# Performance work log

Hardware: AMD Instinct MI355X
Metric: run time of the kernel (lower is better)

The kernel has to match this reference:

```python
import jax, jax.numpy as jnp
import numpy as np

B, N_P, N_S, D, H = 8, 512, 512, 512, 8
HD = D // H
SCALE = HD ** -0.5


def setup_inputs() -> dict:
    key = jax.random.key(0)
    ks = jax.random.split(key, 16)
    init = lambda k, shape, fan_in: jax.random.normal(k, shape, jnp.float32) * (1.0 / np.sqrt(fan_in))
    return {
        "piece_embeds": jax.random.normal(ks[0], (B, N_P, D), jnp.float32),
        "slot_embeds": jax.random.normal(ks[1], (B, N_S, D), jnp.float32),
        "mask": jax.random.randint(ks[2], (B, N_P, N_S), 0, 2, jnp.int32),
        "spatial_bias": jax.random.normal(ks[3], (B, N_P, N_S), jnp.float32),
        "Wq": init(ks[4], (D, D), D), "bq": jnp.zeros((D,), jnp.float32),
        "Wk": init(ks[5], (D, D), D), "bk": jnp.zeros((D,), jnp.float32),
        "Wv": init(ks[6], (D, D), D), "bv": jnp.zeros((D,), jnp.float32),
        "Wo": init(ks[7], (D, D), D), "bo": jnp.zeros((D,), jnp.float32),
        "Wc": init(ks[8], (2 * D,), 2 * D), "bc": jnp.zeros((), jnp.float32),
        "Wval": init(ks[9], (D,), D), "bval": jnp.zeros((), jnp.float32),
    }


def reference(piece_embeds, slot_embeds, mask, spatial_bias,
              Wq, bq, Wk, bk, Wv, bv, Wo, bo, Wc, bc, Wval, bval):
    Bv, Np, Dv = piece_embeds.shape
    Ns = slot_embeds.shape[1]
    Q = (piece_embeds @ Wq + bq).reshape(Bv, Np, H, HD)
    K = (slot_embeds @ Wk + bk).reshape(Bv, Ns, H, HD)
    V = (slot_embeds @ Wv + bv).reshape(Bv, Ns, H, HD)
    # per-head scores, scaled, then averaged over heads (non-standard)
    scores = jnp.einsum('bphd,bshd->bps', Q, K) * (SCALE / H)
    scores = scores + spatial_bias
    scores = jnp.where(mask == 0, jnp.float32(-1e9), scores)
    attn_probs = jax.nn.softmax(scores, axis=-1)  # dropout is identity at eval
    # the original expand*mul*sum over [B,Np,Ns,H,HD] == this contraction
    attn_output = jnp.einsum('bps,bshd->bphd', attn_probs, V).reshape(Bv, Np, Dv)
    output = attn_output @ Wo + bo
    value = (output.mean(axis=1) @ Wval + bval)[:, None]  # [B,1]
    # concat-linear over pairs == split-weight GEMMs with broadcast add
    Wc_p, Wc_s = Wc[:Dv], Wc[Dv:]
    compatibility = (piece_embeds @ Wc_p)[:, :, None] + (slot_embeds @ Wc_s)[:, None, :] + bc
    return scores, value, compatibility
```

## Files before the change

kernel.cpp:

```cpp
#include <hip/hip_runtime.h>
#include <math.h>

#define NP 512
#define NS 512
#define DD 512
#define INV64 0.015625f
#define NEGBIG -1000000000.0f
#define LOG2E 1.4426950408889634f

#define WS_MTBF   0
#define WS_TBF    131072
#define WS_PBF    1179648
#define WS_SBF    2228224
#define WS_WV     3538944
#define WS_U      3539456
#define WS_WQBK   3539968
#define WS_WKBQ   3540480
#define WS_VV     3540992
#define WS_A      3545088
#define WS_E      3549184
#define WS_CP     3553280
#define WS_CS     3557376
#define WS_Z      3561472
#define WS_W      3565568
#define WS_SC     3569664
#define WS_CNT    3569680

#define OUT_SCORES 0
#define OUT_VALUE  2097152
#define OUT_COMP   2097160

typedef short bf16x8 __attribute__((ext_vector_type(8)));
typedef float f32x4 __attribute__((ext_vector_type(4)));

__device__ __forceinline__ short f2bf(float f) {
  unsigned u = __builtin_bit_cast(unsigned, f);
  u += 0x7fffu + ((u >> 16) & 1u);
  return (short)(u >> 16);
}

__device__ __forceinline__ bf16x8 cvt8(float4 a, float4 b) {
  bf16x8 o;
  o[0] = f2bf(a.x); o[1] = f2bf(a.y); o[2] = f2bf(a.z); o[3] = f2bf(a.w);
  o[4] = f2bf(b.x); o[5] = f2bf(b.y); o[6] = f2bf(b.z); o[7] = f2bf(b.w);
  return o;
}

__device__ __forceinline__ void async_copy16(const void* g, void* l) {
  __builtin_amdgcn_global_load_lds(
      (const __attribute__((address_space(1))) unsigned int*)g,
      (__attribute__((address_space(3))) unsigned int*)l, 16, 0, 0);
}

__device__ __forceinline__ float dot8(float4 a0, float4 a1, float4 b0, float4 b1) {
  return a0.x * b0.x + a0.y * b0.y + a0.z * b0.z + a0.w * b0.w +
         a1.x * b1.x + a1.y * b1.y + a1.z * b1.z + a1.w * b1.w;
}

__device__ __forceinline__ float wave_red(float s) {
#pragma unroll
  for (int o = 32; o; o >>= 1) s += __shfl_xor(s, o);
  return s;
}

__device__ inline float wave_dot512(const float* __restrict__ x,
                                    const float* __restrict__ y, int lane) {
  float4 x0 = *(const float4*)&x[lane * 8];
  float4 x1 = *(const float4*)&x[lane * 8 + 4];
  float4 y0 = *(const float4*)&y[lane * 8];
  float4 y1 = *(const float4*)&y[lane * 8 + 4];
  return wave_red(dot8(x0, x1, y0, y1));
}

__global__ __launch_bounds__(256) void kAM(
    const float* __restrict__ Wo, const float* __restrict__ Wval,
    const float* __restrict__ Wq, const float* __restrict__ bk,
    const float* __restrict__ Wk, const float* __restrict__ bq,
    const float* __restrict__ bo, const float* __restrict__ bval,
    float* __restrict__ ws, short* __restrict__ mtb) {
  __shared__ alignas(16) short Asw[2][64 * 72];
  __shared__ alignas(16) short Bsw[2][64 * 72];
  int blk = blockIdx.x;
  if (blk < 385) {
    int wid = blk * 4 + (threadIdx.x >> 6);
    int lane = threadIdx.x & 63;
    if (wid >= 1538) return;
    const float *x, *y;
    float* dst;
    float extra = 0.f;
    int r = wid & 511;
    if (wid < 512)        { x = Wo + (size_t)r * DD; y = Wval; dst = ws + WS_WV + r; }
    else if (wid < 1024)  { x = Wq + (size_t)r * DD; y = bk;   dst = ws + WS_WQBK + r; }
    else if (wid < 1536)  { x = Wk + (size_t)r * DD; y = bq;   dst = ws + WS_WKBQ + r; }
    else if (wid == 1536) { x = bo; y = Wval; dst = ws + WS_SC + 1; extra = *bval; }
    else                  { x = bq; y = bk;   dst = ws + WS_SC + 2; }
    float s = wave_dot512(x, y, lane);
    if (lane == 0) *dst = s + extra;
    return;
  }
  int gb = blk - 385;
  const int m0 = (gb & 7) * 64, n0 = (gb >> 3) * 64;
  const int wave = threadIdx.x >> 6, lane = threadIdx.x & 63;
  const int wr = wave >> 1, wc = wave & 1;
  const int li = lane & 15, g = lane >> 4;
  const int arow = threadIdx.x >> 2, aseg = threadIdx.x & 3;
  f32x4 acc[2][2] = {};

  auto stage = [&](int bufi, int k0) {
    const float* sa = Wk + (size_t)(m0 + arow) * DD + k0 + aseg * 16;
    float4 a0 = *(const float4*)sa, a1 = *(const float4*)(sa + 4);
    float4 a2 = *(const float4*)(sa + 8), a3 = *(const float4*)(sa + 12);
    const float* sb = Wq + (size_t)(n0 + arow) * DD + k0 + aseg * 16;
    float4 b0 = *(const float4*)sb, b1 = *(const float4*)(sb + 4);
    float4 b2 = *(const float4*)(sb + 8), b3 = *(const float4*)(sb + 12);
    *(bf16x8*)&Asw[bufi][arow * 72 + aseg * 16] = cvt8(a0, a1);
    *(bf16x8*)&Asw[bufi][arow * 72 + aseg * 16 + 8] = cvt8(a2, a3);
    *(bf16x8*)&Bsw[bufi][arow * 72 + aseg * 16] = cvt8(b0, b1);
    *(bf16x8*)&Bsw[bufi][arow * 72 + aseg * 16 + 8] = cvt8(b2, b3);
  };

  stage(0, 0);
  __syncthreads();
  int buf = 0;
  for (int k0 = 0; k0 < DD; k0 += 64) {
    if (k0 + 64 < DD) stage(buf ^ 1, k0 + 64);
    bf16x8 af[2][2], bfv[2][2];
#pragma unroll
    for (int kk = 0; kk < 2; ++kk) {
#pragma unroll
      for (int am = 0; am < 2; ++am)
        af[am][kk] = *(const bf16x8*)&Asw[buf][(wr * 32 + am * 16 + li) * 72 + kk * 32 + g * 8];
#pragma unroll
      for (int bn = 0; bn < 2; ++bn)
        bfv[bn][kk] = *(const bf16x8*)&Bsw[buf][(wc * 32 + bn * 16 + li) * 72 + kk * 32 + g * 8];
    }
#pragma unroll
    for (int kk = 0; kk < 2; ++kk)
#pragma unroll
      for (int am = 0; am < 2; ++am)
#pragma unroll
        for (int bn = 0; bn < 2; ++bn)
          acc[am][bn] = __builtin_amdgcn_mfma_f32_16x16x32_bf16(
              af[am][kk], bfv[bn][kk], acc[am][bn], 0, 0, 0);
    __syncthreads();
    buf ^= 1;
  }
#pragma unroll
  for (int am = 0; am < 2; ++am)
#pragma unroll
    for (int i = 0; i < 4; ++i) {
      int grow = m0 + wr * 32 + am * 16 + g * 4 + i;
#pragma unroll
      for (int bn = 0; bn < 2; ++bn) {
        int gcol = n0 + wc * 32 + bn * 16 + li;
        mtb[(size_t)grow * DD + gcol] = f2bf(acc[am][bn][i]);
      }
    }
}

__global__ __launch_bounds__(256) void kCp(
    const float* __restrict__ piece, const float* __restrict__ Wv,
    const float* __restrict__ bv, const float* __restrict__ Wc,
    float* __restrict__ ws, short* __restrict__ pbf, float* __restrict__ out) {
  int lane = threadIdx.x & 63;
  if (blockIdx.x < 1024) {
    int wid = blockIdx.x * 4 + (threadIdx.x >> 6);
    const float* row = piece + (size_t)wid * DD;
    float4 x0 = *(const float4*)&row[lane * 8];
    float4 x1 = *(const float4*)&row[lane * 8 + 4];
    bf16x8 o;
    o[0] = f2bf(x0.x); o[1] = f2bf(x0.y); o[2] = f2bf(x0.z); o[3] = f2bf(x0.w);
    o[4] = f2bf(x1.x); o[5] = f2bf(x1.y); o[6] = f2bf(x1.z); o[7] = f2bf(x1.w);
    *(bf16x8*)&pbf[(size_t)wid * DD + lane * 8] = o;
    const float* y = ws + WS_WQBK;
    float4 y0 = *(const float4*)&y[lane * 8];
    float4 y1 = *(const float4*)&y[lane * 8 + 4];
    float4 c0 = *(const float4*)&Wc[lane * 8];
    float4 c1 = *(const float4*)&Wc[lane * 8 + 4];
    float da = wave_red(dot8(x0, x1, y0, y1));
    float dc = wave_red(dot8(x0, x1, c0, c1));
    if (lane == 0) { ws[WS_A + wid] = da; ws[WS_CP + wid] = dc; }
  } else if (blockIdx.x < 1153) {
    int wid = ((int)blockIdx.x - 1024) * 4 + (threadIdx.x >> 6);
    if (wid > 512) return;
    if (wid < 512) {
      float s = wave_dot512(Wv + (size_t)wid * DD, ws + WS_WV, lane);
      if (lane == 0) ws[WS_U + wid] = s;
    } else {
      float s = wave_dot512(bv, ws + WS_WV, lane);
      if (lane == 0) ws[WS_SC + 0] = s;
    }
  } else {
    float4 zz = make_float4(0.f, 0.f, 0.f, 0.f);
#pragma unroll
    for (int k = 0; k < 8; ++k)
      *(float4*)&ws[WS_Z + (threadIdx.x * 8 + k) * 4] = zz;
    if (threadIdx.x < 64) ((unsigned*)(ws + WS_CNT))[threadIdx.x] = 0u;
    if (threadIdx.x < 8) out[OUT_VALUE + threadIdx.x] = ws[WS_SC + 1];
  }
}

template <int MODE>
__global__ __launch_bounds__(256) void k64(
    const short* __restrict__ A, const short* __restrict__ B,
    short* __restrict__ Cb, const float* __restrict__ slotp,
    const float* __restrict__ Wc, float* __restrict__ ws,
    const float* __restrict__ sbias, const int* __restrict__ maskp,
    const float* __restrict__ bc, float* __restrict__ out,
    short* __restrict__ sbf) {
  __shared__ alignas(16) short SH[4][4096];
  __shared__ unsigned tick;
  const int wave = threadIdx.x >> 6, lane = threadIdx.x & 63;
  const int id = blockIdx.x;

  if (MODE == 1 && id >= 512) {
    int wid = (id - 512) * 4 + wave;
    const float* row = slotp + (size_t)wid * DD;
    float4 x0 = *(const float4*)&row[lane * 8];
    float4 x1 = *(const float4*)&row[lane * 8 + 4];
    bf16x8 o;
    o[0] = f2bf(x0.x); o[1] = f2bf(x0.y); o[2] = f2bf(x0.z); o[3] = f2bf(x0.w);
    o[4] = f2bf(x1.x); o[5] = f2bf(x1.y); o[6] = f2bf(x1.z); o[7] = f2bf(x1.w);
    *(bf16x8*)&sbf[(size_t)wid * DD + lane * 8] = o;
    const float* y = ws + WS_WKBQ;
    float4 y0 = *(const float4*)&y[lane * 8];
    float4 y1 = *(const float4*)&y[lane * 8 + 4];
    const float* u = ws + WS_U;
    float4 u0 = *(const float4*)&u[lane * 8];
    float4 u1 = *(const float4*)&u[lane * 8 + 4];
    const float* c = Wc + DD;
    float4 c0 = *(const float4*)&c[lane * 8];
    float4 c1 = *(const float4*)&c[lane * 8 + 4];
    float de = wave_red(dot8(x0, x1, y0, y1));
    float dv = wave_red(dot8(x0, x1, u0, u1));
    float dc = wave_red(dot8(x0, x1, c0, c1));
    if (lane == 0) {
      ws[WS_E + wid] = de;
      ws[WS_VV + wid] = dv + ws[WS_SC + 0];
      ws[WS_CS + wid] = dc;
    }
    return;
  }

  const int wr = wave >> 1, wc = wave & 1;
  const int li = lane & 15, g = lane >> 4;
  int b = 0, m0, n0;
  if (MODE == 1) { m0 = (id & 63) * 64; n0 = (id >> 6) * 64; }
  else           { b = id & 7; m0 = ((id >> 6) & 7) * 64; n0 = ((id >> 3) & 7) * 64; }
  const short* Ab = A + (size_t)b * NP * DD;
  const short* Bb = B + (size_t)b * NS * DD;
  f32x4 acc[2][2] = {};
  float4 sb4r[4];
  int4 mk4r[4];
  const int er = threadIdx.x >> 2, eq = threadIdx.x & 3;
  const size_t ebase = ((size_t)b * NP + m0 + er) * NS + n0 + eq * 16;

  auto stage = [&](int bufi, int k0) {
#pragma unroll
    for (int h = 0; h < 2; ++h) {
      int s = h * 256 + threadIdx.x;
      int row = s >> 3;
      int gsrc = (s & 7) ^ (row & 7);
      async_copy16(Ab + (size_t)(m0 + row) * DD + k0 + gsrc * 8, &SH[bufi][s * 8]);
      async_copy16(Bb + (size_t)(n0 + row) * DD + k0 + gsrc * 8, &SH[2 + bufi][s * 8]);
    }
  };

  stage(0, 0);
  __syncthreads();
  int buf = 0;
  for (int k0 = 0; k0 < DD; k0 += 64) {
    if (k0 + 64 < DD) stage(buf ^ 1, k0 + 64);
    if (MODE == 2) {
      if (k0 == 256) {
#pragma unroll
        for (int h = 0; h < 4; ++h)
          sb4r[h] = *(const float4*)&sbias[ebase + h * 4];
      } else if (k0 == 384) {
#pragma unroll
        for (int h = 0; h < 4; ++h)
          mk4r[h] = *(const int4*)&maskp[ebase + h * 4];
      }
    }
    bf16x8 af[2][2], bfv[2][2];
#pragma unroll
    for (int kk = 0; kk < 2; ++kk) {
#pragma unroll
      for (int am = 0; am < 2; ++am) {
        int row = wr * 32 + am * 16 + li;
        af[am][kk] = *(const bf16x8*)&SH[buf][(row * 8 + ((kk * 4 + g) ^ (row & 7))) * 8];
      }
#pragma unroll
      for (int bn = 0; bn < 2; ++bn) {
        int row = wc * 32 + bn * 16 + li;
        bfv[bn][kk] = *(const bf16x8*)&SH[2 + buf][(row * 8 + ((kk * 4 + g) ^ (row & 7))) * 8];
      }
    }
#pragma unroll
    for (int kk = 0; kk < 2; ++kk)
#pragma unroll
      for (int am = 0; am < 2; ++am)
#pragma unroll
        for (int bn = 0; bn < 2; ++bn)
          acc[am][bn] = __builtin_amdgcn_mfma_f32_16x16x32_bf16(
              af[am][kk], bfv[bn][kk], acc[am][bn], 0, 0, 0);
    if (k0 + 64 < DD) {
      __syncthreads();
      buf ^= 1;
    }
  }
  __syncthreads();

  if (MODE == 1) {
    short* cs = &SH[0][0];
#pragma unroll
    for (int am = 0; am < 2; ++am)
#pragma unroll
      for (int i = 0; i < 4; ++i) {
        int row = wr * 32 + am * 16 + g * 4 + i;
#pragma unroll
        for (int bn = 0; bn < 2; ++bn)
          cs[row * 68 + wc * 32 + bn * 16 + li] = f2bf(acc[am][bn][i]);
      }
    __syncthreads();
    int r = threadIdx.x >> 2, q = threadIdx.x & 3;
#pragma unroll
    for (int h = 0; h < 2; ++h) {
      bf16x8 v = *(const bf16x8*)&cs[r * 68 + q * 16 + h * 8];
      *(bf16x8*)&Cb[(size_t)(m0 + r) * DD + n0 + q * 16 + h * 8] = v;
    }
  } else {
    float* cf = (float*)&SH[0][0];
#pragma unroll
    for (int am = 0; am < 2; ++am)
#pragma unroll
      for (int i = 0; i < 4; ++i) {
        int row = wr * 32 + am * 16 + g * 4 + i;
#pragma unroll
        for (int bn = 0; bn < 2; ++bn)
          cf[row * 68 + wc * 32 + bn * 16 + li] = acc[am][bn][i];
      }
    __syncthreads();
    const float sbb = ws[WS_SC + 2];
    const float bcv = *bc;
    int p = m0 + er;
    float av = ws[WS_A + b * NP + p] + sbb;
    float cpv = ws[WS_CP + b * NP + p] + bcv;
    float zp = 0.f, wp = 0.f;
#pragma unroll
    for (int h = 0; h < 4; ++h) {
      int c = eq * 16 + h * 4;
      int scol = n0 + c;
      size_t idx = ebase + h * 4;
      float4 a4 = *(const float4*)&cf[er * 68 + c];
      float4 sb4 = sb4r[h];
      int4 mk4 = mk4r[h];
      float4 e4 = *(const float4*)&ws[WS_E + b * NS + scol];
      float4 vv4 = *(const float4*)&ws[WS_VV + b * NS + scol];
      float4 cs4 = *(const float4*)&ws[WS_CS + b * NS + scol];
      float4 v;
      v.x = (mk4.x == 0) ? NEGBIG : fmaf(a4.x + av + e4.x, INV64, sb4.x);
      v.y = (mk4.y == 0) ? NEGBIG : fmaf(a4.y + av + e4.y, INV64, sb4.y);
      v.z = (mk4.z == 0) ? NEGBIG : fmaf(a4.z + av + e4.z, INV64, sb4.z);
      v.w = (mk4.w == 0) ? NEGBIG : fmaf(a4.w + av + e4.w, INV64, sb4.w);
      *(float4*)&out[OUT_SCORES + idx] = v;
      float e;
      e = exp2f(v.x * LOG2E); zp += e; wp += e * vv4.x;
      e = exp2f(v.y * LOG2E); zp += e; wp += e * vv4.y;
      e = exp2f(v.z * LOG2E); zp += e; wp += e * vv4.z;
      e = exp2f(v.w * LOG2E); zp += e; wp += e * vv4.w;
      float4 cm = make_float4(cpv + cs4.x, cpv + cs4.y, cpv + cs4.z, cpv + cs4.w);
      *(float4*)&out[OUT_COMP + idx] = cm;
    }
    zp += __shfl_xor(zp, 1); zp += __shfl_xor(zp, 2);
    wp += __shfl_xor(wp, 1); wp += __shfl_xor(wp, 2);
    if (eq == 0) {
      atomicAdd(&ws[WS_Z + b * NP + p], zp);
      atomicAdd(&ws[WS_W + b * NP + p], wp);
    }
    __syncthreads();
    if (threadIdx.x == 0)
      tick = atomicAdd((unsigned*)(ws + WS_CNT) + (b * 8 + ((id >> 6) & 7)), 1u);
    __syncthreads();
    if (tick == 7 && threadIdx.x < 64) {
      int pr = m0 + threadIdx.x;
      float zz = atomicAdd(&ws[WS_Z + b * NP + pr], 0.0f);
      float ww = atomicAdd(&ws[WS_W + b * NP + pr], 0.0f);
      float v = wave_red(ww / zz);
      if (threadIdx.x == 0) atomicAdd(&out[OUT_VALUE + b], v * (1.0f / NP));
    }
  }
}

extern "C" void kernel_launch(void* const* d_in, const int* in_sizes, int n_in,
                              void* d_out, int out_size, void* d_ws,
                              size_t ws_size, hipStream_t stream) {
  const float* piece = (const float*)d_in[0];
  const float* slot = (const float*)d_in[1];
  const int* mask = (const int*)d_in[2];
  const float* sbias = (const float*)d_in[3];
  const float* Wq = (const float*)d_in[4];
  const float* bq = (const float*)d_in[5];
  const float* Wk = (const float*)d_in[6];
  const float* bk = (const float*)d_in[7];
  const float* Wv = (const float*)d_in[8];
  const float* bv = (const float*)d_in[9];
  const float* Wo = (const float*)d_in[10];
  const float* bo = (const float*)d_in[11];
  const float* Wc = (const float*)d_in[12];
  const float* bc = (const float*)d_in[13];
  const float* Wval = (const float*)d_in[14];
  const float* bval = (const float*)d_in[15];
  float* out = (float*)d_out;
  float* ws = (float*)d_ws;

  short* mtb = (short*)(ws + WS_MTBF);
  short* tbf = (short*)(ws + WS_TBF);
  short* pbf = (short*)(ws + WS_PBF);
  short* sbf = (short*)(ws + WS_SBF);

  hipLaunchKernelGGL(kAM, dim3(449), dim3(256), 0, stream,
                     Wo, Wval, Wq, bk, Wk, bq, bo, bval, ws, mtb);
  hipLaunchKernelGGL(kCp, dim3(1154), dim3(256), 0, stream,
                     piece, Wv, bv, Wc, ws, pbf, out);
  hipLaunchKernelGGL((k64<1>), dim3(1536), dim3(256), 0, stream,
                     pbf, mtb, tbf, slot, Wc, ws,
                     (const float*)nullptr, (const int*)nullptr,
                     (const float*)nullptr, (float*)nullptr, sbf);
  hipLaunchKernelGGL((k64<2>), dim3(512), dim3(256), 0, stream,
                     tbf, sbf, (short*)nullptr, (const float*)nullptr,
                     (const float*)nullptr, ws, sbias, mask, bc, out,
                     (short*)nullptr);
}
```

Baseline: 43.11 us.

## Fuse fp32-to-bf16 input conversion and row dot products into GEMM kernels

```diff
diff --git a/kernel.cpp b/kernel.cpp
--- a/kernel.cpp
+++ b/kernel.cpp
@@ -10,21 +10,16 @@
 
 #define WS_MTBF   0
 #define WS_TBF    131072
-#define WS_PBF    1179648
-#define WS_SBF    2228224
-#define WS_WV     3538944
-#define WS_U      3539456
-#define WS_WQBK   3539968
-#define WS_WKBQ   3540480
-#define WS_VV     3540992
-#define WS_A      3545088
-#define WS_E      3549184
-#define WS_CP     3553280
-#define WS_CS     3557376
-#define WS_Z      3561472
-#define WS_W      3565568
-#define WS_SC     3569664
-#define WS_CNT    3569680
+#define WS_WV     1179648
+#define WS_U      1180160
+#define WS_WQBK   1180672
+#define WS_WKBQ   1181184
+#define WS_A      1181696
+#define WS_CP     1185792
+#define WS_Z      1189888
+#define WS_W      1193984
+#define WS_SC     1198080
+#define WS_CNT    1198096
 
 #define OUT_SCORES 0
 #define OUT_VALUE  2097152
@@ -158,111 +153,66 @@
     }
 }
 
-__global__ __launch_bounds__(256) void kCp(
-    const float* __restrict__ piece, const float* __restrict__ Wv,
-    const float* __restrict__ bv, const float* __restrict__ Wc,
-    float* __restrict__ ws, short* __restrict__ pbf, float* __restrict__ out) {
-  int lane = threadIdx.x & 63;
-  if (blockIdx.x < 1024) {
-    int wid = blockIdx.x * 4 + (threadIdx.x >> 6);
-    const float* row = piece + (size_t)wid * DD;
-    float4 x0 = *(const float4*)&row[lane * 8];
-    float4 x1 = *(const float4*)&row[lane * 8 + 4];
-    bf16x8 o;
-    o[0] = f2bf(x0.x); o[1] = f2bf(x0.y); o[2] = f2bf(x0.z); o[3] = f2bf(x0.w);
-    o[4] = f2bf(x1.x); o[5] = f2bf(x1.y); o[6] = f2bf(x1.z); o[7] = f2bf(x1.w);
-    *(bf16x8*)&pbf[(size_t)wid * DD + lane * 8] = o;
-    const float* y = ws + WS_WQBK;
-    float4 y0 = *(const float4*)&y[lane * 8];
-    float4 y1 = *(const float4*)&y[lane * 8 + 4];
-    float4 c0 = *(const float4*)&Wc[lane * 8];
-    float4 c1 = *(const float4*)&Wc[lane * 8 + 4];
-    float da = wave_red(dot8(x0, x1, y0, y1));
-    float dc = wave_red(dot8(x0, x1, c0, c1));
-    if (lane == 0) { ws[WS_A + wid] = da; ws[WS_CP + wid] = dc; }
-  } else if (blockIdx.x < 1153) {
-    int wid = ((int)blockIdx.x - 1024) * 4 + (threadIdx.x >> 6);
-    if (wid > 512) return;
-    if (wid < 512) {
-      float s = wave_dot512(Wv + (size_t)wid * DD, ws + WS_WV, lane);
-      if (lane == 0) ws[WS_U + wid] = s;
+__global__ __launch_bounds__(256) void kT(
+    const float* __restrict__ piece, const short* __restrict__ mtb,
+    const float* __restrict__ Wv, const float* __restrict__ bv,
+    const float* __restrict__ Wc, float* __restrict__ ws,
+    short* __restrict__ tbf, float* __restrict__ out) {
+  __shared__ alignas(16) short Asw[2][64 * 72];
+  __shared__ alignas(16) short Bsg[2][64 * 64];
+  const int id = blockIdx.x;
+  const int wave = threadIdx.x >> 6, lane = threadIdx.x & 63;
+
+  if (id >= 512) {
+    if (id < 641) {
+      int wid = (id - 512) * 4 + wave;
+      if (wid > 512) return;
+      if (wid < 512) {
+        float s = wave_dot512(Wv + (size_t)wid * DD, ws + WS_WV, lane);
+        if (lane == 0) ws[WS_U + wid] = s;
+      } else {
+        float s = wave_dot512(bv, ws + WS_WV, lane);
+        if (lane == 0) ws[WS_SC + 0] = s;
+      }
     } else {
-      float s = wave_dot512(bv, ws + WS_WV, lane);
-      if (lane == 0) ws[WS_SC + 0] = s;
-    }
-  } else {
-    float4 zz = make_float4(0.f, 0.f, 0.f, 0.f);
-#pragma unroll
-    for (int k = 0; k < 8; ++k)
-      *(float4*)&ws[WS_Z + (threadIdx.x * 8 + k) * 4] = zz;
-    if (threadIdx.x < 64) ((unsigned*)(ws + WS_CNT))[threadIdx.x] = 0u;
-    if (threadIdx.x < 8) out[OUT_VALUE + threadIdx.x] = ws[WS_SC + 1];
-  }
-}
-
-template <int MODE>
-__global__ __launch_bounds__(256) void k64(
-    const short* __restrict__ A, const short* __restrict__ B,
-    short* __restrict__ Cb, const float* __restrict__ slotp,
-    const float* __restrict__ Wc, float* __restrict__ ws,
-    const float* __restrict__ sbias, const int* __restrict__ maskp,
-    const float* __restrict__ bc, float* __restrict__ out,
-    short* __restrict__ sbf) {
-  __shared__ alignas(16) short SH[4][4096];
-  __shared__ unsigned tick;
-  const int wave = threadIdx.x >> 6, lane = threadIdx.x & 63;
-  const int id = blockIdx.x;
-
-  if (MODE == 1 && id >= 512) {
-    int wid = (id - 512) * 4 + wave;
-    const float* row = slotp + (size_t)wid * DD;
-    float4 x0 = *(const float4*)&row[lane * 8];
-    float4 x1 = *(const float4*)&row[lane * 8 + 4];
-    bf16x8 o;
-    o[0] = f2bf(x0.x); o[1] = f2bf(x0.y); o[2] = f2bf(x0.z); o[3] = f2bf(x0.w);
-    o[4] = f2bf(x1.x); o[5] = f2bf(x1.y); o[6] = f2bf(x1.z); o[7] = f2bf(x1.w);
-    *(bf16x8*)&sbf[(size_t)wid * DD + lane * 8] = o;
-    const float* y = ws + WS_WKBQ;
-    float4 y0 = *(const float4*)&y[lane * 8];
-    float4 y1 = *(const float4*)&y[lane * 8 + 4];
-    const float* u = ws + WS_U;
-    float4 u0 = *(const float4*)&u[lane * 8];
-    float4 u1 = *(const float4*)&u[lane * 8 + 4];
-    const float* c = Wc + DD;
-    float4 c0 = *(const float4*)&c[lane * 8];
-    float4 c1 = *(const float4*)&c[lane * 8 + 4];
-    float de = wave_red(dot8(x0, x1, y0, y1));
-    float dv = wave_red(dot8(x0, x1, u0, u1));
-    float dc = wave_red(dot8(x0, x1, c0, c1));
-    if (lane == 0) {
-      ws[WS_E + wid] = de;
-      ws[WS_VV + wid] = dv + ws[WS_SC + 0];
-      ws[WS_CS + wid] = dc;
+      float4 zz = make_float4(0.f, 0.f, 0.f, 0.f);
+#pragma unroll
+      for (int k = 0; k < 8; ++k)
+        *(float4*)&ws[WS_Z + (threadIdx.x * 8 + k) * 4] = zz;
+      if (threadIdx.x < 64) ((unsigned*)(ws + WS_CNT))[threadIdx.x] = 0u;
+      if (threadIdx.x < 8) out[OUT_VALUE + threadIdx.x] = ws[WS_SC + 1];
     }
     return;
   }
 
   const int wr = wave >> 1, wc = wave & 1;
   const int li = lane & 15, g = lane >> 4;
-  int b = 0, m0, n0;
-  if (MODE == 1) { m0 = (id & 63) * 64; n0 = (id >> 6) * 64; }
-  else           { b = id & 7; m0 = ((id >> 6) & 7) * 64; n0 = ((id >> 3) & 7) * 64; }
-  const short* Ab = A + (size_t)b * NP * DD;
-  const short* Bb = B + (size_t)b * NS * DD;
+  const int m0 = (id & 63) * 64, n0 = (id >> 6) * 64;
+  const int arow = threadIdx.x >> 2, aseg = threadIdx.x & 3;
+  const bool do_dots = (n0 == 0);
+  float a_acc = 0.f, cp_acc = 0.f;
   f32x4 acc[2][2] = {};
-  float4 sb4r[4];
-  int4 mk4r[4];
-  const int er = threadIdx.x >> 2, eq = threadIdx.x & 3;
-  const size_t ebase = ((size_t)b * NP + m0 + er) * NS + n0 + eq * 16;
 
   auto stage = [&](int bufi, int k0) {
+    const float* sa = piece + (size_t)(m0 + arow) * DD + k0 + aseg * 16;
+    float4 a0 = *(const float4*)sa, a1 = *(const float4*)(sa + 4);
+    float4 a2 = *(const float4*)(sa + 8), a3 = *(const float4*)(sa + 12);
 #pragma unroll
     for (int h = 0; h < 2; ++h) {
       int s = h * 256 + threadIdx.x;
       int row = s >> 3;
       int gsrc = (s & 7) ^ (row & 7);
-      async_copy16(Ab + (size_t)(m0 + row) * DD + k0 + gsrc * 8, &SH[bufi][s * 8]);
-      async_copy16(Bb + (size_t)(n0 + row) * DD + k0 + gsrc * 8, &SH[2 + bufi][s * 8]);
+      async_copy16(mtb + (size_t)(n0 + row) * DD + k0 + gsrc * 8, &Bsg[bufi][s * 8]);
+    }
+    *(bf16x8*)&Asw[bufi][arow * 72 + aseg * 16] = cvt8(a0, a1);
+    *(bf16x8*)&Asw[bufi][arow * 72 + aseg * 16 + 8] = cvt8(a2, a3);
+    if (do_dots) {
+      const float* yq = ws + WS_WQBK + k0 + aseg * 16;
+      const float* yc = Wc + k0 + aseg * 16;
+      a_acc += dot8(a0, a1, *(const float4*)yq, *(const float4*)(yq + 4)) +
+               dot8(a2, a3, *(const float4*)(yq + 8), *(const float4*)(yq + 12));
+      cp_acc += dot8(a0, a1, *(const float4*)yc, *(const float4*)(yc + 4)) +
+                dot8(a2, a3, *(const float4*)(yc + 8), *(const float4*)(yc + 12));
     }
   };
 
@@ -271,29 +221,16 @@
   int buf = 0;
   for (int k0 = 0; k0 < DD; k0 += 64) {
     if (k0 + 64 < DD) stage(buf ^ 1, k0 + 64);
-    if (MODE == 2) {
-      if (k0 == 256) {
-#pragma unroll
-        for (int h = 0; h < 4; ++h)
-          sb4r[h] = *(const float4*)&sbias[ebase + h * 4];
-      } else if (k0 == 384) {
-#pragma unroll
-        for (int h = 0; h < 4; ++h)
-          mk4r[h] = *(const int4*)&maskp[ebase + h * 4];
-      }
-    }
     bf16x8 af[2][2], bfv[2][2];
 #pragma unroll
     for (int kk = 0; kk < 2; ++kk) {
 #pragma unroll
-      for (int am = 0; am < 2; ++am) {
-        int row = wr * 32 + am * 16 + li;
-        af[am][kk] = *(const bf16x8*)&SH[buf][(row * 8 + ((kk * 4 + g) ^ (row & 7))) * 8];
-      }
+      for (int am = 0; am < 2; ++am)
+        af[am][kk] = *(const bf16x8*)&Asw[buf][(wr * 32 + am * 16 + li) * 72 + kk * 32 + g * 8];
 #pragma unroll
       for (int bn = 0; bn < 2; ++bn) {
         int row = wc * 32 + bn * 16 + li;
-        bfv[bn][kk] = *(const bf16x8*)&SH[2 + buf][(row * 8 + ((kk * 4 + g) ^ (row & 7))) * 8];
+        bfv[bn][kk] = *(const bf16x8*)&Bsg[buf][(row * 8 + ((kk * 4 + g) ^ (row & 7))) * 8];
       }
     }
 #pragma unroll
@@ -309,86 +246,188 @@
       buf ^= 1;
     }
   }
-  __syncthreads();
-
-  if (MODE == 1) {
-    short* cs = &SH[0][0];
-#pragma unroll
-    for (int am = 0; am < 2; ++am)
-#pragma unroll
-      for (int i = 0; i < 4; ++i) {
-        int row = wr * 32 + am * 16 + g * 4 + i;
+  if (do_dots) {
+    a_acc += __shfl_xor(a_acc, 1);  a_acc += __shfl_xor(a_acc, 2);
+    cp_acc += __shfl_xor(cp_acc, 1); cp_acc += __shfl_xor(cp_acc, 2);
+    if (aseg == 0) {
+      ws[WS_A + m0 + arow] = a_acc;
+      ws[WS_CP + m0 + arow] = cp_acc;
+    }
+  }
+  __syncthreads();
+  short* cs = &Asw[0][0];
+#pragma unroll
+  for (int am = 0; am < 2; ++am)
+#pragma unroll
+    for (int i = 0; i < 4; ++i) {
+      int row = wr * 32 + am * 16 + g * 4 + i;
+#pragma unroll
+      for (int bn = 0; bn < 2; ++bn)
+        cs[row * 68 + wc * 32 + bn * 16 + li] = f2bf(acc[am][bn][i]);
+    }
+  __syncthreads();
+  int r = threadIdx.x >> 2, q = threadIdx.x & 3;
+#pragma unroll
+  for (int h = 0; h < 2; ++h) {
+    bf16x8 v = *(const bf16x8*)&cs[r * 68 + q * 16 + h * 8];
+    *(bf16x8*)&tbf[(size_t)(m0 + r) * DD + n0 + q * 16 + h * 8] = v;
+  }
+}
+
+__global__ __launch_bounds__(256) void kS(
+    const short* __restrict__ tbf, const float* __restrict__ slotp,
+    const float* __restrict__ Wc, float* __restrict__ ws,
+    const float* __restrict__ sbias, const int* __restrict__ maskp,
+    const float* __restrict__ bc, float* __restrict__ out) {
+  __shared__ alignas(16) short Asg[2][64 * 64];
+  __shared__ alignas(16) short Bsw[2][64 * 72];
+  __shared__ alignas(16) float e_l[64];
+  __shared__ alignas(16) float vv_l[64];
+  __shared__ alignas(16) float cs_l[64];
+  __shared__ unsigned tick;
+  const int id = blockIdx.x;
+  const int wave = threadIdx.x >> 6, lane = threadIdx.x & 63;
+  const int wr = wave >> 1, wc = wave & 1;
+  const int li = lane & 15, g = lane >> 4;
+  const int b = id & 7, m0 = ((id >> 6) & 7) * 64, n0 = ((id >> 3) & 7) * 64;
+  const short* Ab = tbf + (size_t)b * NP * DD;
+  const int brow = threadIdx.x >> 2, bseg = threadIdx.x & 3;
+  float e_acc = 0.f, vv_acc = 0.f, cs_acc = 0.f;
+  f32x4 acc[2][2] = {};
+  float4 sb4r[4];
+  int4 mk4r[4];
+  const int er = threadIdx.x >> 2, eq = threadIdx.x & 3;
+  const size_t ebase = ((size_t)b * NP + m0 + er) * NS + n0 + eq * 16;
+
+  auto stage = [&](int bufi, int k0) {
+    const float* sb = slotp + (size_t)(b * NS + n0 + brow) * DD + k0 + bseg * 16;
+    float4 b0 = *(const float4*)sb, b1 = *(const float4*)(sb + 4);
+    float4 b2 = *(const float4*)(sb + 8), b3 = *(const float4*)(sb + 12);
+#pragma unroll
+    for (int h = 0; h < 2; ++h) {
+      int s = h * 256 + threadIdx.x;
+      int row = s >> 3;
+      int gsrc = (s & 7) ^ (row & 7);
+      async_copy16(Ab + (size_t)(m0 + row) * DD + k0 + gsrc * 8, &Asg[bufi][s * 8]);
+    }
+    *(bf16x8*)&Bsw[bufi][brow * 72 + bseg * 16] = cvt8(b0, b1);
+    *(bf16x8*)&Bsw[bufi][brow * 72 + bseg * 16 + 8] = cvt8(b2, b3);
+    const float* yk = ws + WS_WKBQ + k0 + bseg * 16;
+    const float* yu = ws + WS_U + k0 + bseg * 16;
+    const float* yc = Wc + DD + k0 + bseg * 16;
+    e_acc += dot8(b0, b1, *(const float4*)yk, *(const float4*)(yk + 4)) +
+             dot8(b2, b3, *(const float4*)(yk + 8), *(const float4*)(yk + 12));
+    vv_acc += dot8(b0, b1, *(const float4*)yu, *(const float4*)(yu + 4)) +
+              dot8(b2, b3, *(const float4*)(yu + 8), *(const float4*)(yu + 12));
+    cs_acc += dot8(b0, b1, *(const float4*)yc, *(const float4*)(yc + 4)) +
+              dot8(b2, b3, *(const float4*)(yc + 8), *(const float4*)(yc + 12));
+  };
+
+  stage(0, 0);
+  __syncthreads();
+  int buf = 0;
+  for (int k0 = 0; k0 < DD; k0 += 64) {
+    if (k0 + 64 < DD) stage(buf ^ 1, k0 + 64);
+    if (k0 == 256) {
+#pragma unroll
+      for (int h = 0; h < 4; ++h) sb4r[h] = *(const float4*)&sbias[ebase + h * 4];
+    } else if (k0 == 384) {
+#pragma unroll
+      for (int h = 0; h < 4; ++h) mk4r[h] = *(const int4*)&maskp[ebase + h * 4];
+    }
+    bf16x8 af[2][2], bfv[2][2];
+#pragma unroll
+    for (int kk = 0; kk < 2; ++kk) {
+#pragma unroll
+      for (int am = 0; am < 2; ++am) {
+        int row = wr * 32 + am * 16 + li;
+        af[am][kk] = *(const bf16x8*)&Asg[buf][(row * 8 + ((kk * 4 + g) ^ (row & 7))) * 8];
+      }
+#pragma unroll
+      for (int bn = 0; bn < 2; ++bn)
+        bfv[bn][kk] = *(const bf16x8*)&Bsw[buf][(wc * 32 + bn * 16 + li) * 72 + kk * 32 + g * 8];
+    }
+#pragma unroll
+    for (int kk = 0; kk < 2; ++kk)
+#pragma unroll
+      for (int am = 0; am < 2; ++am)
 #pragma unroll
         for (int bn = 0; bn < 2; ++bn)
-          cs[row * 68 + wc * 32 + bn * 16 + li] = f2bf(acc[am][bn][i]);
-      }
-    __syncthreads();
-    int r = threadIdx.x >> 2, q = threadIdx.x & 3;
-#pragma unroll
-    for (int h = 0; h < 2; ++h) {
-      bf16x8 v = *(const bf16x8*)&cs[r * 68 + q * 16 + h * 8];
-      *(bf16x8*)&Cb[(size_t)(m0 + r) * DD + n0 + q * 16 + h * 8] = v;
-    }
-  } else {
-    float* cf = (float*)&SH[0][0];
-#pragma unroll
-    for (int am = 0; am < 2; ++am)
-#pragma unroll
-      for (int i = 0; i < 4; ++i) {
-        int row = wr * 32 + am * 16 + g * 4 + i;
-#pragma unroll
-        for (int bn = 0; bn < 2; ++bn)
-          cf[row * 68 + wc * 32 + bn * 16 + li] = acc[am][bn][i];
-      }
-    __syncthreads();
-    const float sbb = ws[WS_SC + 2];
-    const float bcv = *bc;
-    int p = m0 + er;
-    float av = ws[WS_A + b * NP + p] + sbb;
-    float cpv = ws[WS_CP + b * NP + p] + bcv;
-    float zp = 0.f, wp = 0.f;
-#pragma unroll
-    for (int h = 0; h < 4; ++h) {
-      int c = eq * 16 + h * 4;
-      int scol = n0 + c;
-      size_t idx = ebase + h * 4;
-      float4 a4 = *(const float4*)&cf[er * 68 + c];
-      float4 sb4 = sb4r[h];
-      int4 mk4 = mk4r[h];
-      float4 e4 = *(const float4*)&ws[WS_E + b * NS + scol];
-      float4 vv4 = *(const float4*)&ws[WS_VV + b * NS + scol];
-      float4 cs4 = *(const float4*)&ws[WS_CS + b * NS + scol];
-      float4 v;
-      v.x = (mk4.x == 0) ? NEGBIG : fmaf(a4.x + av + e4.x, INV64, sb4.x);
-      v.y = (mk4.y == 0) ? NEGBIG : fmaf(a4.y + av + e4.y, INV64, sb4.y);
-      v.z = (mk4.z == 0) ? NEGBIG : fmaf(a4.z + av + e4.z, INV64, sb4.z);
-      v.w = (mk4.w == 0) ? NEGBIG : fmaf(a4.w + av + e4.w, INV64, sb4.w);
-      *(float4*)&out[OUT_SCORES + idx] = v;
-      float e;
-      e = exp2f(v.x * LOG2E); zp += e; wp += e * vv4.x;
-      e = exp2f(v.y * LOG2E); zp += e; wp += e * vv4.y;
-      e = exp2f(v.z * LOG2E); zp += e; wp += e * vv4.z;
-      e = exp2f(v.w * LOG2E); zp += e; wp += e * vv4.w;
-      float4 cm = make_float4(cpv + cs4.x, cpv + cs4.y, cpv + cs4.z, cpv + cs4.w);
-      *(float4*)&out[OUT_COMP + idx] = cm;
-    }
-    zp += __shfl_xor(zp, 1); zp += __shfl_xor(zp, 2);
-    wp += __shfl_xor(wp, 1); wp += __shfl_xor(wp, 2);
-    if (eq == 0) {
-      atomicAdd(&ws[WS_Z + b * NP + p], zp);
-      atomicAdd(&ws[WS_W + b * NP + p], wp);
-    }
-    __syncthreads();
-    if (threadIdx.x == 0)
-      tick = atomicAdd((unsigned*)(ws + WS_CNT) + (b * 8 + ((id >> 6) & 7)), 1u);
-    __syncthreads();
-    if (tick == 7 && threadIdx.x < 64) {
-      int pr = m0 + threadIdx.x;
-      float zz = atomicAdd(&ws[WS_Z + b * NP + pr], 0.0f);
-      float ww = atomicAdd(&ws[WS_W + b * NP + pr], 0.0f);
-      float v = wave_red(ww / zz);
-      if (threadIdx.x == 0) atomicAdd(&out[OUT_VALUE + b], v * (1.0f / NP));
-    }
+          acc[am][bn] = __builtin_amdgcn_mfma_f32_16x16x32_bf16(
+              af[am][kk], bfv[bn][kk], acc[am][bn], 0, 0, 0);
+    if (k0 + 64 < DD) {
+      __syncthreads();
+      buf ^= 1;
+    }
+  }
+
+  e_acc += __shfl_xor(e_acc, 1); e_acc += __shfl_xor(e_acc, 2);
+  vv_acc += __shfl_xor(vv_acc, 1); vv_acc += __shfl_xor(vv_acc, 2);
+  cs_acc += __shfl_xor(cs_acc, 1); cs_acc += __shfl_xor(cs_acc, 2);
+  if (bseg == 0) {
+    e_l[brow] = e_acc;
+    vv_l[brow] = vv_acc + ws[WS_SC + 0];
+    cs_l[brow] = cs_acc;
+  }
+  __syncthreads();
+
+  float* cf = (float*)&Bsw[0][0];
+#pragma unroll
+  for (int am = 0; am < 2; ++am)
+#pragma unroll
+    for (int i = 0; i < 4; ++i) {
+      int row = wr * 32 + am * 16 + g * 4 + i;
+#pragma unroll
+      for (int bn = 0; bn < 2; ++bn)
+        cf[row * 68 + wc * 32 + bn * 16 + li] = acc[am][bn][i];
+    }
+  __syncthreads();
+  const float sbb = ws[WS_SC + 2];
+  const float bcv = *bc;
+  int p = m0 + er;
+  float av = ws[WS_A + b * NP + p] + sbb;
+  float cpv = ws[WS_CP + b * NP + p] + bcv;
+  float zp = 0.f, wp = 0.f;
+#pragma unroll
+  for (int h = 0; h < 4; ++h) {
+    int c = eq * 16 + h * 4;
+    size_t idx = ebase + h * 4;
+    float4 a4 = *(const float4*)&cf[er * 68 + c];
+    float4 sb4 = sb4r[h];
+    int4 mk4 = mk4r[h];
+    float4 e4 = *(const float4*)&e_l[c];
+    float4 vv4 = *(const float4*)&vv_l[c];
+    float4 cs4 = *(const float4*)&cs_l[c];
+    float4 v;
+    v.x = (mk4.x == 0) ? NEGBIG : fmaf(a4.x + av + e4.x, INV64, sb4.x);
+    v.y = (mk4.y == 0) ? NEGBIG : fmaf(a4.y + av + e4.y, INV64, sb4.y);
+    v.z = (mk4.z == 0) ? NEGBIG : fmaf(a4.z + av + e4.z, INV64, sb4.z);
+    v.w = (mk4.w == 0) ? NEGBIG : fmaf(a4.w + av + e4.w, INV64, sb4.w);
+    *(float4*)&out[OUT_SCORES + idx] = v;
+    float e;
+    e = exp2f(v.x * LOG2E); zp += e; wp += e * vv4.x;
+    e = exp2f(v.y * LOG2E); zp += e; wp += e * vv4.y;
+    e = exp2f(v.z * LOG2E); zp += e; wp += e * vv4.z;
+    e = exp2f(v.w * LOG2E); zp += e; wp += e * vv4.w;
+    float4 cm = make_float4(cpv + cs4.x, cpv + cs4.y, cpv + cs4.z, cpv + cs4.w);
+    *(float4*)&out[OUT_COMP + idx] = cm;
+  }
+  zp += __shfl_xor(zp, 1); zp += __shfl_xor(zp, 2);
+  wp += __shfl_xor(wp, 1); wp += __shfl_xor(wp, 2);
+  if (eq == 0) {
+    atomicAdd(&ws[WS_Z + b * NP + p], zp);
+    atomicAdd(&ws[WS_W + b * NP + p], wp);
+  }
+  __syncthreads();
+  if (threadIdx.x == 0)
+    tick = atomicAdd((unsigned*)(ws + WS_CNT) + (b * 8 + ((id >> 6) & 7)), 1u);
+  __syncthreads();
+  if (tick == 7 && threadIdx.x < 64) {
+    int pr = m0 + threadIdx.x;
+    float zz = atomicAdd(&ws[WS_Z + b * NP + pr], 0.0f);
+    float ww = atomicAdd(&ws[WS_W + b * NP + pr], 0.0f);
+    float v = wave_red(ww / zz);
+    if (threadIdx.x == 0) atomicAdd(&out[OUT_VALUE + b], v * (1.0f / NP));
   }
 }
 
@@ -416,19 +455,11 @@
 
   short* mtb = (short*)(ws + WS_MTBF);
   short* tbf = (short*)(ws + WS_TBF);
-  short* pbf = (short*)(ws + WS_PBF);
-  short* sbf = (short*)(ws + WS_SBF);
 
   hipLaunchKernelGGL(kAM, dim3(449), dim3(256), 0, stream,
                      Wo, Wval, Wq, bk, Wk, bq, bo, bval, ws, mtb);
-  hipLaunchKernelGGL(kCp, dim3(1154), dim3(256), 0, stream,
-                     piece, Wv, bv, Wc, ws, pbf, out);
-  hipLaunchKernelGGL((k64<1>), dim3(1536), dim3(256), 0, stream,
-                     pbf, mtb, tbf, slot, Wc, ws,
-                     (const float*)nullptr, (const int*)nullptr,
-                     (const float*)nullptr, (float*)nullptr, sbf);
-  hipLaunchKernelGGL((k64<2>), dim3(512), dim3(256), 0, stream,
-                     tbf, sbf, (short*)nullptr, (const float*)nullptr,
-                     (const float*)nullptr, ws, sbias, mask, bc, out,
-                     (short*)nullptr);
-}
+  hipLaunchKernelGGL(kT, dim3(642), dim3(256), 0, stream,
+                     piece, mtb, Wv, bv, Wc, ws, tbf, out);
+  hipLaunchKernelGGL(kS, dim3(512), dim3(256), 0, stream,
+                     tbf, slot, Wc, ws, sbias, mask, bc, out);
+}
```

After: 56.38 us. 1.31x slower.

## Move piece bf16 conversion into first kernel and compute A-dots from bf16 copy

Applied to the files above, without the earlier changes.

```diff
diff --git a/kernel.cpp b/kernel.cpp
--- a/kernel.cpp
+++ b/kernel.cpp
@@ -39,6 +39,11 @@
   return (short)(u >> 16);
 }
 
+__device__ __forceinline__ float bf2f(short s) {
+  unsigned u = ((unsigned)(unsigned short)s) << 16;
+  return __builtin_bit_cast(float, u);
+}
+
 __device__ __forceinline__ bf16x8 cvt8(float4 a, float4 b) {
   bf16x8 o;
   o[0] = f2bf(a.x); o[1] = f2bf(a.y); o[2] = f2bf(a.z); o[3] = f2bf(a.w);
@@ -77,13 +82,14 @@
     const float* __restrict__ Wq, const float* __restrict__ bk,
     const float* __restrict__ Wk, const float* __restrict__ bq,
     const float* __restrict__ bo, const float* __restrict__ bval,
-    float* __restrict__ ws, short* __restrict__ mtb) {
+    const float* __restrict__ piece, const float* __restrict__ Wc,
+    float* __restrict__ ws, short* __restrict__ mtb, short* __restrict__ pbf) {
   __shared__ alignas(16) short Asw[2][64 * 72];
   __shared__ alignas(16) short Bsw[2][64 * 72];
   int blk = blockIdx.x;
+  const int wave = threadIdx.x >> 6, lane = threadIdx.x & 63;
   if (blk < 385) {
-    int wid = blk * 4 + (threadIdx.x >> 6);
-    int lane = threadIdx.x & 63;
+    int wid = blk * 4 + wave;
     if (wid >= 1538) return;
     const float *x, *y;
     float* dst;
@@ -98,9 +104,20 @@
     if (lane == 0) *dst = s + extra;
     return;
   }
+  if (blk >= 449) {
+    int wid = (blk - 449) * 4 + wave;
+    const float* row = piece + (size_t)wid * DD;
+    float4 x0 = *(const float4*)&row[lane * 8];
+    float4 x1 = *(const float4*)&row[lane * 8 + 4];
+    *(bf16x8*)&pbf[(size_t)wid * DD + lane * 8] = cvt8(x0, x1);
+    float4 c0 = *(const float4*)&Wc[lane * 8];
+    float4 c1 = *(const float4*)&Wc[lane * 8 + 4];
+    float dc = wave_red(dot8(x0, x1, c0, c1));
+    if (lane == 0) ws[WS_CP + wid] = dc;
+    return;
+  }
   int gb = blk - 385;
   const int m0 = (gb & 7) * 64, n0 = (gb >> 3) * 64;
-  const int wave = threadIdx.x >> 6, lane = threadIdx.x & 63;
   const int wr = wave >> 1, wc = wave & 1;
   const int li = lane & 15, g = lane >> 4;
   const int arow = threadIdx.x >> 2, aseg = threadIdx.x & 3;
@@ -158,30 +175,14 @@
     }
 }
 
-__global__ __launch_bounds__(256) void kCp(
-    const float* __restrict__ piece, const float* __restrict__ Wv,
-    const float* __restrict__ bv, const float* __restrict__ Wc,
-    float* __restrict__ ws, short* __restrict__ pbf, float* __restrict__ out) {
-  int lane = threadIdx.x & 63;
-  if (blockIdx.x < 1024) {
-    int wid = blockIdx.x * 4 + (threadIdx.x >> 6);
-    const float* row = piece + (size_t)wid * DD;
-    float4 x0 = *(const float4*)&row[lane * 8];
-    float4 x1 = *(const float4*)&row[lane * 8 + 4];
-    bf16x8 o;
-    o[0] = f2bf(x0.x); o[1] = f2bf(x0.y); o[2] = f2bf(x0.z); o[3] = f2bf(x0.w);
-    o[4] = f2bf(x1.x); o[5] = f2bf(x1.y); o[6] = f2bf(x1.z); o[7] = f2bf(x1.w);
-    *(bf16x8*)&pbf[(size_t)wid * DD + lane * 8] = o;
-    const float* y = ws + WS_WQBK;
-    float4 y0 = *(const float4*)&y[lane * 8];
-    float4 y1 = *(const float4*)&y[lane * 8 + 4];
-    float4 c0 = *(const float4*)&Wc[lane * 8];
-    float4 c1 = *(const float4*)&Wc[lane * 8 + 4];
-    float da = wave_red(dot8(x0, x1, y0, y1));
-    float dc = wave_red(dot8(x0, x1, c0, c1));
-    if (lane == 0) { ws[WS_A + wid] = da; ws[WS_CP + wid] = dc; }
-  } else if (blockIdx.x < 1153) {
-    int wid = ((int)blockIdx.x - 1024) * 4 + (threadIdx.x >> 6);
+__global__ __launch_bounds__(256) void kU(
+    const float* __restrict__ Wv, const float* __restrict__ bv,
+    float* __restrict__ ws, const short* __restrict__ pbf,
+    float* __restrict__ out) {
+  const int wave = threadIdx.x >> 6, lane = threadIdx.x & 63;
+  int blk = blockIdx.x;
+  if (blk < 129) {
+    int wid = blk * 4 + wave;
     if (wid > 512) return;
     if (wid < 512) {
       float s = wave_dot512(Wv + (size_t)wid * DD, ws + WS_WV, lane);
@@ -189,6 +190,20 @@
     } else {
       float s = wave_dot512(bv, ws + WS_WV, lane);
       if (lane == 0) ws[WS_SC + 0] = s;
+    }
+  } else if (blk < 385) {
+    const float* y = ws + WS_WQBK;
+    float4 y0 = *(const float4*)&y[lane * 8];
+    float4 y1 = *(const float4*)&y[lane * 8 + 4];
+    int base = (((blk - 129) * 4 + wave)) * 4;
+#pragma unroll
+    for (int r = 0; r < 4; ++r) {
+      int row = base + r;
+      bf16x8 v = *(const bf16x8*)&pbf[(size_t)row * DD + lane * 8];
+      float4 x0 = make_float4(bf2f(v[0]), bf2f(v[1]), bf2f(v[2]), bf2f(v[3]));
+      float4 x1 = make_float4(bf2f(v[4]), bf2f(v[5]), bf2f(v[6]), bf2f(v[7]));
+      float s = wave_red(dot8(x0, x1, y0, y1));
+      if (lane == 0) ws[WS_A + row] = s;
     }
   } else {
     float4 zz = make_float4(0.f, 0.f, 0.f, 0.f);
@@ -218,10 +233,7 @@
     const float* row = slotp + (size_t)wid * DD;
     float4 x0 = *(const float4*)&row[lane * 8];
     float4 x1 = *(const float4*)&row[lane * 8 + 4];
-    bf16x8 o;
-    o[0] = f2bf(x0.x); o[1] = f2bf(x0.y); o[2] = f2bf(x0.z); o[3] = f2bf(x0.w);
-    o[4] = f2bf(x1.x); o[5] = f2bf(x1.y); o[6] = f2bf(x1.z); o[7] = f2bf(x1.w);
-    *(bf16x8*)&sbf[(size_t)wid * DD + lane * 8] = o;
+    *(bf16x8*)&sbf[(size_t)wid * DD + lane * 8] = cvt8(x0, x1);
     const float* y = ws + WS_WKBQ;
     float4 y0 = *(const float4*)&y[lane * 8];
     float4 y1 = *(const float4*)&y[lane * 8 + 4];
@@ -274,12 +286,10 @@
     if (MODE == 2) {
       if (k0 == 256) {
 #pragma unroll
-        for (int h = 0; h < 4; ++h)
-          sb4r[h] = *(const float4*)&sbias[ebase + h * 4];
+        for (int h = 0; h < 4; ++h) sb4r[h] = *(const float4*)&sbias[ebase + h * 4];
       } else if (k0 == 384) {
 #pragma unroll
-        for (int h = 0; h < 4; ++h)
-          mk4r[h] = *(const int4*)&maskp[ebase + h * 4];
+        for (int h = 0; h < 4; ++h) mk4r[h] = *(const int4*)&maskp[ebase + h * 4];
       }
     }
     bf16x8 af[2][2], bfv[2][2];
@@ -419,10 +429,9 @@
   short* pbf = (short*)(ws + WS_PBF);
   short* sbf = (short*)(ws + WS_SBF);
 
-  hipLaunchKernelGGL(kAM, dim3(449), dim3(256), 0, stream,
-                     Wo, Wval, Wq, bk, Wk, bq, bo, bval, ws, mtb);
-  hipLaunchKernelGGL(kCp, dim3(1154), dim3(256), 0, stream,
-                     piece, Wv, bv, Wc, ws, pbf, out);
+  hipLaunchKernelGGL(kAM, dim3(1473), dim3(256), 0, stream,
+                     Wo, Wval, Wq, bk, Wk, bq, bo, bval, piece, Wc, ws, mtb, pbf);
+  hipLaunchKernelGGL(kU, dim3(386), dim3(256), 0, stream, Wv, bv, ws, pbf, out);
   hipLaunchKernelGGL((k64<1>), dim3(1536), dim3(256), 0, stream,
                      pbf, mtb, tbf, slot, Wc, ws,
                      (const float*)nullptr, (const int*)nullptr,
```

New measurement: 44.29 us. 1.03x slower.
